# Performance work log

Measured on AMD Instinct MI355X. Metric: run time of the kernel, lower is better.

## Reference

```python
import jax, jax.numpy as jnp
import numpy as np

NUM_HEADS = 16
BUDGET = 1024


def layer_norm(x, g, b, eps=1e-5):
    mu = jnp.mean(x, axis=-1, keepdims=True)
    var = jnp.mean((x - mu) ** 2, axis=-1, keepdims=True)
    return (x - mu) / jnp.sqrt(var + eps) * g + b


def setup_inputs() -> dict:
    key = jax.random.key(0)
    ks = jax.random.split(key, 6)
    B, N, D = 2, 2048, 1024
    H, Dh = NUM_HEADS, 1024 // NUM_HEADS
    sc = 1.0 / np.sqrt(D).astype(np.float32)
    X = jax.random.normal(ks[0], (B, N, D), jnp.float32)
    W_q = jax.random.normal(ks[1], (D, D), jnp.float32) * sc
    W_k = jax.random.normal(ks[2], (D, D), jnp.float32) * sc
    W_v = jax.random.normal(ks[3], (D, D), jnp.float32) * sc
    W_o = jax.random.normal(ks[4], (D, D), jnp.float32) * sc
    return dict(
        X=X, W_q=W_q, W_k=W_k, W_v=W_v, W_o=W_o,
        gamma_q=jnp.ones((D,), jnp.float32), beta_q=jnp.zeros((D,), jnp.float32),
        gamma_k=jnp.ones((D,), jnp.float32), beta_k=jnp.zeros((D,), jnp.float32),
        cache_k=jnp.zeros((B, H, BUDGET, Dh), jnp.float32),
        cache_v=jnp.zeros((B, H, BUDGET, Dh), jnp.float32),
        start_pos=0,
    )


def reference(X, W_q, W_k, W_v, W_o, gamma_q, beta_q, gamma_k, beta_k,
              cache_k, cache_v, start_pos):
    B, N, D = X.shape
    H = NUM_HEADS
    Dh = D // H
    budget = cache_k.shape[2]
    M = start_pos + N  # total kv length

    XQ = layer_norm(X @ W_q, gamma_q, beta_q).reshape(B, N, H, Dh).transpose(0, 2, 1, 3)
    XK = layer_norm(X @ W_k, gamma_k, beta_k).reshape(B, N, H, Dh).transpose(0, 2, 1, 3)
    XV = (X @ W_v).reshape(B, N, H, Dh).transpose(0, 2, 1, 3)

    K = jnp.concatenate([cache_k[:B, :, :start_pos], XK], axis=2)  # (B,H,M,Dh)
    V = jnp.concatenate([cache_v[:B, :, :start_pos], XV], axis=2)

    logits = jnp.einsum('bhnd,bhmd->bhnm', XQ, K) / np.float32(np.sqrt(Dh))
    n_idx = jnp.arange(N)[:, None]
    m_idx = jnp.arange(M)[None, :]
    causal_keep = (m_idx < start_pos) | ((m_idx - start_pos) <= n_idx)  # (N,M)
    logits = jnp.where(causal_keep, logits, -jnp.inf)

    # --- selection (eviction) scores from head 0 ---
    S = jax.nn.relu(logits[:, 0])                        # (B,N,M); relu(-inf)=0
    S = S.at[:, :, start_pos].set(0.0)                   # never evict <BOS>-like slot
    S = S.at[:, :, start_pos:].multiply(1.0 - jnp.eye(N, dtype=S.dtype))  # zero diagonal
    S = jnp.roll(S, 1, axis=1).at[:, 0, :].set(0.0)      # shift: scores apply from next query
    Fm = jnp.cumsum(S, axis=1)                           # (B,N,M) cumulative eviction scores

    # --- sequential heavy-hitter eviction ---
    unmasked0 = jnp.broadcast_to(jnp.arange(budget, dtype=jnp.int32), (B, budget))
    kpos = jnp.arange(budget, dtype=jnp.int32)[None, :]

    def step(unmasked, i):
        new_idx = jnp.concatenate(
            [unmasked, jnp.full((B, 1), i, unmasked.dtype)], axis=1)     # (B,budget+1)
        row = jax.lax.dynamic_index_in_dim(Fm, i - start_pos, axis=1, keepdims=False)  # (B,M)
        scores = jnp.take_along_axis(row, new_idx, axis=1)
        idx = jnp.argmax(scores, axis=-1)                                # (B,)
        evicted = jnp.take_along_axis(new_idx, idx[:, None], axis=1)[:, 0]
        unmasked = jnp.where(kpos < idx[:, None], new_idx[:, :budget], new_idx[:, 1:])
        return unmasked, evicted

    steps = jnp.arange(max(budget, start_pos), M, dtype=jnp.int32)       # (T,)
    _, evicts = jax.lax.scan(step, unmasked0, steps)                     # evicts (T,B)

    big = jnp.int32(M + start_pos + 1)
    evict_time = jnp.full((B, M), big, jnp.int32)
    evict_time = evict_time.at[jnp.arange(B, dtype=jnp.int32)[None, :], evicts].min(steps[:, None])
    # query row j is pruned from key m iff (j + start_pos) >= evict_time[m]
    prune_keep = (jnp.arange(N)[:, None] + start_pos) < evict_time[:, None, :]  # (B,N,M)

    logits = jnp.where(prune_keep[:, None], logits, -jnp.inf)
    attn = jax.nn.softmax(logits, axis=-1)
    O = jnp.einsum('bhnm,bhmd->bhnd', attn, V).transpose(0, 2, 1, 3).reshape(B, N, D)
    return O @ W_o
```

## Files before the change

kernel.cpp:

```cpp
#include <hip/hip_runtime.h>

#define B_    2
#define N_    2048
#define D_    1024
#define H_    16
#define DH_   64
#define M_    2048
#define ROWS_ 4096
#define BUD_  1024

typedef unsigned short u16;
typedef unsigned int   u32;
typedef unsigned long long u64;
typedef __attribute__((ext_vector_type(8))) short short8;
typedef __attribute__((ext_vector_type(4))) float floatx4;

__device__ __forceinline__ u16 f2b(float f) {
    u32 u = __float_as_uint(f);
    return (u16)((u + 0x7FFFu + ((u >> 16) & 1u)) >> 16);
}
__device__ __forceinline__ float b2f(u16 h) {
    return __uint_as_float(((u32)h) << 16);
}

__global__ __launch_bounds__(256) void cast_x_kernel(
    const float* __restrict__ X, u16* __restrict__ Xhi, u16* __restrict__ Xlo)
{
    int idx = (blockIdx.x * 256 + threadIdx.x) * 4;
    float4 v = *(const float4*)&X[idx];
    u16 h0 = f2b(v.x), h1 = f2b(v.y), h2 = f2b(v.z), h3 = f2b(v.w);
    ushort4 hv; hv.x = h0; hv.y = h1; hv.z = h2; hv.w = h3;
    *(ushort4*)&Xhi[idx] = hv;
    ushort4 lv;
    lv.x = f2b(v.x - b2f(h0)); lv.y = f2b(v.y - b2f(h1));
    lv.z = f2b(v.z - b2f(h2)); lv.w = f2b(v.w - b2f(h3));
    *(ushort4*)&Xlo[idx] = lv;
}

__global__ __launch_bounds__(1024) void cast_w_kernel(
    const float* __restrict__ W, u16* __restrict__ Whi, u16* __restrict__ Wlo,
    int do_lo)
{
    __shared__ float tile[32][33];
    int tx = threadIdx.x, ty = threadIdx.y;
    int x = blockIdx.x * 32 + tx, y = blockIdx.y * 32 + ty;
    tile[ty][tx] = W[(size_t)y * D_ + x];
    __syncthreads();
    float v = tile[tx][ty];
    int n = blockIdx.x * 32 + ty, k = blockIdx.y * 32 + tx;
    u16 h = f2b(v);
    Whi[(size_t)n * D_ + k] = h;
    if (do_lo) Wlo[(size_t)n * D_ + k] = f2b(v - b2f(h));
}

__global__ __launch_bounds__(256) void gemm_kernel(
    const u16* __restrict__ Ah, const u16* __restrict__ Al,
    const u16* __restrict__ Bh, const u16* __restrict__ Bl,
    int mode, float* __restrict__ C)
{
    __shared__ __align__(16) u16 sAh[128 * 32];
    __shared__ __align__(16) u16 sBh[128 * 32];
    __shared__ __align__(16) u16 sAl[128 * 32];
    __shared__ __align__(16) u16 sBl[128 * 32];
    int tid = threadIdx.x;
    int lane = tid & 63, wv = tid >> 6;
    int wr = wv >> 1, wc = wv & 1;
    int quad = lane >> 4, l16 = lane & 15;
    int m0 = blockIdx.y * 128, n0 = blockIdx.x * 128;

    floatx4 acc[4][4];
    floatx4 zero = {0.f, 0.f, 0.f, 0.f};
#pragma unroll
    for (int i = 0; i < 4; ++i)
#pragma unroll
        for (int j = 0; j < 4; ++j) acc[i][j] = zero;

    for (int k0 = 0; k0 < 1024; k0 += 32) {
#pragma unroll
        for (int it = 0; it < 2; ++it) {
            int e = (tid + it * 256) * 8;
            int r = e >> 5, c = e & 31;
            *(uint4*)&sAh[e] = *(const uint4*)&Ah[(size_t)(m0 + r) * 1024 + k0 + c];
            *(uint4*)&sBh[e] = *(const uint4*)&Bh[(size_t)(n0 + r) * 1024 + k0 + c];
            if (mode) {
                *(uint4*)&sAl[e] = *(const uint4*)&Al[(size_t)(m0 + r) * 1024 + k0 + c];
                *(uint4*)&sBl[e] = *(const uint4*)&Bl[(size_t)(n0 + r) * 1024 + k0 + c];
            }
        }
        __syncthreads();
        short8 ah[4], al[4], bh[4], bl[4];
#pragma unroll
        for (int x = 0; x < 4; ++x) {
            int ra = (wr * 64 + x * 16 + l16) * 32 + quad * 8;
            int rb = (wc * 64 + x * 16 + l16) * 32 + quad * 8;
            ah[x] = *(const short8*)&sAh[ra];
            bh[x] = *(const short8*)&sBh[rb];
            if (mode) {
                al[x] = *(const short8*)&sAl[ra];
                bl[x] = *(const short8*)&sBl[rb];
            }
        }
#pragma unroll
        for (int mi = 0; mi < 4; ++mi)
#pragma unroll
            for (int ni = 0; ni < 4; ++ni) {
                acc[mi][ni] = __builtin_amdgcn_mfma_f32_16x16x32_bf16(
                    ah[mi], bh[ni], acc[mi][ni], 0, 0, 0);
                if (mode) {
                    acc[mi][ni] = __builtin_amdgcn_mfma_f32_16x16x32_bf16(
                        ah[mi], bl[ni], acc[mi][ni], 0, 0, 0);
                    acc[mi][ni] = __builtin_amdgcn_mfma_f32_16x16x32_bf16(
                        al[mi], bh[ni], acc[mi][ni], 0, 0, 0);
                }
            }
        __syncthreads();
    }
#pragma unroll
    for (int mi = 0; mi < 4; ++mi)
#pragma unroll
        for (int ni = 0; ni < 4; ++ni)
#pragma unroll
            for (int r = 0; r < 4; ++r) {
                int row = m0 + wr * 64 + mi * 16 + quad * 4 + r;
                int col = n0 + wc * 64 + ni * 16 + l16;
                C[(size_t)row * 1024 + col] = acc[mi][ni][r];
            }
}

__global__ __launch_bounds__(256) void lnpack_kernel(
    const float* __restrict__ Y, const float* __restrict__ gamma,
    const float* __restrict__ beta, u16* __restrict__ Pk,
    float* __restrict__ head0, int do_ln)
{
    int r = blockIdx.x;
    int tid = threadIdx.x;
    float4 v = *(const float4*)&Y[(size_t)r * D_ + tid * 4];
    float mu = 0.f, rsig = 1.f;
    __shared__ float sS[4], sQ[4];
    if (do_ln) {
        float s = v.x + v.y + v.z + v.w;
        float q = v.x * v.x + v.y * v.y + v.z * v.z + v.w * v.w;
#pragma unroll
        for (int d = 1; d < 64; d <<= 1) { s += __shfl_xor(s, d); q += __shfl_xor(q, d); }
        if ((tid & 63) == 0) { sS[tid >> 6] = s; sQ[tid >> 6] = q; }
        __syncthreads();
        s = sS[0] + sS[1] + sS[2] + sS[3];
        q = sQ[0] + sQ[1] + sQ[2] + sQ[3];
        mu = s * (1.f / 1024.f);
        float var = q * (1.f / 1024.f) - mu * mu;
        rsig = rsqrtf(var + 1e-5f);
    }
    int b = r >> 11, n = r & 2047;
    float xs[4] = {v.x, v.y, v.z, v.w};
#pragma unroll
    for (int j = 0; j < 4; ++j) {
        int c = tid * 4 + j;
        float val = do_ln ? ((xs[j] - mu) * rsig * gamma[c] + beta[c]) : xs[j];
        int h = c >> 6, dh = c & 63;
        Pk[(((size_t)b * H_ + h) * N_ + n) * DH_ + dh] = f2b(val);
        if (head0 && c < 64) head0[(size_t)r * 64 + c] = val;
    }
}

__global__ void s_kernel(const float* __restrict__ q0,
                         const float* __restrict__ k0, float* __restrict__ S)
{
    int b = blockIdx.z;
    int n0 = blockIdx.y * 16, m0 = blockIdx.x * 16;
    int tx = threadIdx.x, ty = threadIdx.y;
    int n = n0 + ty, m = m0 + tx;
    float* out = S + ((size_t)b * N_ + n) * M_ + m;
    if (m0 > n0 + 15) { *out = 0.f; return; }
    __shared__ float sq[16][65], sk[16][65];
    int tid = ty * 16 + tx;
    {
        int rr = tid >> 4, cc = (tid & 15) * 4;
        float4 qa = *(const float4*)&q0[((size_t)b * N_ + n0 + rr) * 64 + cc];
        sq[rr][cc] = qa.x; sq[rr][cc + 1] = qa.y; sq[rr][cc + 2] = qa.z; sq[rr][cc + 3] = qa.w;
        float4 ka = *(const float4*)&k0[((size_t)b * N_ + m0 + rr) * 64 + cc];
        sk[rr][cc] = ka.x; sk[rr][cc + 1] = ka.y; sk[rr][cc + 2] = ka.z; sk[rr][cc + 3] = ka.w;
    }
    __syncthreads();
    float acc = 0.f;
#pragma unroll 8
    for (int d = 0; d < 64; ++d) acc += sq[ty][d] * sk[tx][d];
    float val;
    if (m < n && m != 0) val = fmaxf(acc * 0.125f, 0.f); else val = 0.f;
    *out = val;
}

__global__ __launch_bounds__(256) void p_kernel(const float* __restrict__ S,
                                                float* __restrict__ P)
{
    int b = blockIdx.z, c = blockIdx.y;
    int m = blockIdx.x * 256 + threadIdx.x;
    const float* base = S + ((size_t)b * N_ + c * 128) * M_ + m;
    float s = 0.f;
    for (int j = 0; j < 128; ++j) s += base[(size_t)j * M_];
    P[((size_t)b * 8 + c) * M_ + m] = s;
}

__device__ __forceinline__ void vsel(float& va, u32& la, float vb, u32 lb) {
    bool tk = vb > va;
    va = tk ? vb : va;
    la = tk ? lb : la;
}

template<int CTRL, int RMASK>
__device__ __forceinline__ void dpp_max_pack(float& v, u32& lo) {
    int hi = __float_as_int(v);
    int hi_o = __builtin_amdgcn_update_dpp(hi, hi, CTRL, RMASK, 0xF, false);
    int lo_o = __builtin_amdgcn_update_dpp((int)lo, (int)lo, CTRL, RMASK, 0xF, false);
    long long a = (long long)((((u64)(u32)hi) << 32) | lo);
    long long b = (long long)((((u64)(u32)hi_o) << 32) | (u32)lo_o);
    bool tk = b > a;
    v = tk ? __int_as_float(hi_o) : v;
    lo = tk ? (u32)lo_o : lo;
}

__device__ __forceinline__ void wave_argmax_to63(float& v, u32& lo) {
    dpp_max_pack<0x121, 0xF>(v, lo);
    dpp_max_pack<0x122, 0xF>(v, lo);
    dpp_max_pack<0x124, 0xF>(v, lo);
    dpp_max_pack<0x128, 0xF>(v, lo);
    dpp_max_pack<0x142, 0xA>(v, lo);
    dpp_max_pack<0x143, 0xC>(v, lo);
}

#define GLOAD(dst, voff, ptr, imm)                                    \
    asm volatile("global_load_dwordx4 %0, %1, %2 offset:" #imm        \
                 : "=v"(dst) : "v"(voff), "s"(ptr) : "memory")

#define ISSUE2(bank, row)                                             \
    {                                                                 \
        u32 r_ = (u32)((row) < 2047 ? (row) : 2047);                  \
        u32 vo = wbyte + r_ * 8192u;                                  \
        GLOAD(bank[0], vo, Sb, 0);                                    \
        GLOAD(bank[1], vo, Sb, 1024);                                 \
    }

#define VWAIT6()                                                      \
    do { asm volatile("s_waitcnt vmcnt(6)" ::: "memory");             \
         __builtin_amdgcn_sched_barrier(0); } while (0)
#define VWAIT0()                                                      \
    do { asm volatile("s_waitcnt vmcnt(0)" ::: "memory");             \
         __builtin_amdgcn_sched_barrier(0); } while (0)

__device__ __forceinline__ void evict_step4(
    int i, int t, int w, int par,
    const u32 (&lov)[2][4], float (&cum)[2][4], int (&evti)[2][4],
    const floatx4 (&bank)[2], uint2 (*spair)[4])
{
    const float NEGINF = __uint_as_float(0xFF800000u);
    float v0 = cum[0][0]; u32 l0 = lov[0][0];
    vsel(v0, l0, cum[0][1], lov[0][1]);
    float v1 = cum[0][2]; u32 l1 = lov[0][2];
    vsel(v1, l1, cum[0][3], lov[0][3]);
    vsel(v0, l0, v1, l1);
    float v2 = cum[1][0]; u32 l2 = lov[1][0];
    vsel(v2, l2, cum[1][1], lov[1][1]);
    float v3 = cum[1][2]; u32 l3 = lov[1][2];
    vsel(v3, l3, cum[1][3], lov[1][3]);
    vsel(v2, l2, v3, l3);
    vsel(v0, l0, v2, l2);
    wave_argmax_to63(v0, l0);
    if (t == 63) spair[par][w] = make_uint2(l0, (u32)__float_as_int(v0));
    asm volatile("s_waitcnt lgkmcnt(0)" ::: "memory");
    __builtin_amdgcn_sched_barrier(0);
    __builtin_amdgcn_s_barrier();
    __builtin_amdgcn_sched_barrier(0);
    uint2 q0 = spair[par][0], q1 = spair[par][1];
    uint2 q2 = spair[par][2], q3 = spair[par][3];
    long long k0 = (long long)((((u64)q0.y) << 32) | q0.x);
    long long k1 = (long long)((((u64)q1.y) << 32) | q1.x);
    long long k2 = (long long)((((u64)q2.y) << 32) | q2.x);
    long long k3 = (long long)((((u64)q3.y) << 32) | q3.x);
    long long ba = k0 > k1 ? k0 : k1;
    long long bb = k2 > k3 ? k2 : k3;
    long long bst = ba > bb ? ba : bb;
    const u32 lostar = (u32)(bst & 0xFFFFFFFFll);
#pragma unroll
    for (int c = 0; c < 2; ++c) {
        cum[c][0] += bank[c][0]; cum[c][1] += bank[c][1];
        cum[c][2] += bank[c][2]; cum[c][3] += bank[c][3];
    }
#pragma unroll
    for (int c = 0; c < 2; ++c)
#pragma unroll
        for (int e = 0; e < 4; ++e) {
            bool hit = (lov[c][e] == lostar);
            cum[c][e] = hit ? NEGINF : cum[c][e];
            evti[c][e] = hit ? i : evti[c][e];
        }
}

__device__ void evict_role(const float* __restrict__ S,
                           const float* __restrict__ P,
                           int* __restrict__ evt)
{
    int b = blockIdx.x;
    int tid = threadIdx.x;
    int w = tid >> 6, t = tid & 63;
    const float* Sb = S + (size_t)b * N_ * M_;
    int* evtb = evt + b * M_;
    const int mbase = 512 * w + 4 * t;
    const u32 wbyte = (u32)(2048 * w + 16 * t);
    __shared__ uint2 spair[2][4];
    u32 lov[2][4];
    int evti[2][4];
#pragma unroll
    for (int c = 0; c < 2; ++c)
#pragma unroll
        for (int e = 0; e < 4; ++e) {
            lov[c][e] = (u32)(2048 - (mbase + 256 * c + e));
            evti[c][e] = 0x3FFFFFFF;
        }
    float cum[2][4];
#pragma unroll
    for (int c = 0; c < 2; ++c) {
        float ax = 0.f, ay = 0.f, az = 0.f, aw = 0.f;
#pragma unroll
        for (int cc = 0; cc < 8; ++cc) {
            floatx4 pv = *(const floatx4*)&P[((size_t)b * 8 + cc) * M_ + mbase + 256 * c];
            ax += pv[0]; ay += pv[1]; az += pv[2]; aw += pv[3];
        }
        cum[c][0] = ax; cum[c][1] = ay; cum[c][2] = az; cum[c][3] = aw;
    }
    VWAIT0();
    floatx4 bA[2], bB[2], bC[2], bD[2];
    ISSUE2(bA, 1024)
    ISSUE2(bB, 1025)
    ISSUE2(bC, 1026)
    ISSUE2(bD, 1027)
#pragma unroll 1
    for (int ip = 1024; ip < 2048; ip += 4) {
        VWAIT6();
        evict_step4(ip + 0, t, w, 0, lov, cum, evti, bA, spair);
        ISSUE2(bA, ip + 4)
        VWAIT6();
        evict_step4(ip + 1, t, w, 1, lov, cum, evti, bB, spair);
        ISSUE2(bB, ip + 5)
        VWAIT6();
        evict_step4(ip + 2, t, w, 0, lov, cum, evti, bC, spair);
        ISSUE2(bC, ip + 6)
        VWAIT6();
        evict_step4(ip + 3, t, w, 1, lov, cum, evti, bD, spair);
        ISSUE2(bD, ip + 7)
    }
    VWAIT0();
#pragma unroll
    for (int c = 0; c < 2; ++c) {
        int4 o; o.x = evti[c][0]; o.y = evti[c][1];
        o.z = evti[c][2]; o.w = evti[c][3];
        *(int4*)&evtb[mbase + 256 * c] = o;
    }
}

__device__ void flash_role(
    const u16* __restrict__ Qb, const u16* __restrict__ Kb,
    const u16* __restrict__ Vb, const int* __restrict__ evtg,
    u16* __restrict__ Ob, int bh, int q0, int ktiles)
{
    int b = bh >> 4, h = bh & 15;
    int tid = threadIdx.x, lane = tid & 63, w = tid >> 6;
    int quad = lane >> 4, l16 = lane & 15;
    const u16* Qh = Qb + (size_t)bh * N_ * DH_;
    const u16* Kh = Kb + (size_t)bh * N_ * DH_;
    const u16* Vh = Vb + (size_t)bh * N_ * DH_;
    __shared__ __align__(16) u16 sK[64 * 64];
    __shared__ __align__(16) u16 sV[64 * 64];
    __shared__ __align__(16) u16 sP[4][16 * 64];
    __shared__ int sevt[64];

    short8 aq0 = *(const short8*)&Qh[(size_t)(q0 + w * 16 + l16) * 64 + quad * 8];
    short8 aq1 = *(const short8*)&Qh[(size_t)(q0 + w * 16 + l16) * 64 + quad * 8 + 32];

    floatx4 zero = {0.f, 0.f, 0.f, 0.f};
    floatx4 accO[4];
#pragma unroll
    for (int d = 0; d < 4; ++d) accO[d] = zero;
    float m_i[4] = {-1e30f, -1e30f, -1e30f, -1e30f};
    float l_i[4] = {0.f, 0.f, 0.f, 0.f};

    for (int kt = 0; kt < ktiles; ++kt) {
        int k0 = kt * 64;
#pragma unroll
        for (int it = 0; it < 2; ++it) {
            int e = (tid + it * 256) * 8;
            int r = e >> 6, c = e & 63;
            *(uint4*)&sK[e] = *(const uint4*)&Kh[(size_t)(k0 + r) * 64 + c];
            uint4 vv = *(const uint4*)&Vh[(size_t)(k0 + r) * 64 + c];
            sV[(c + 0) * 64 + r] = (u16)(vv.x & 0xFFFF);
            sV[(c + 1) * 64 + r] = (u16)(vv.x >> 16);
            sV[(c + 2) * 64 + r] = (u16)(vv.y & 0xFFFF);
            sV[(c + 3) * 64 + r] = (u16)(vv.y >> 16);
            sV[(c + 4) * 64 + r] = (u16)(vv.z & 0xFFFF);
            sV[(c + 5) * 64 + r] = (u16)(vv.z >> 16);
            sV[(c + 6) * 64 + r] = (u16)(vv.w & 0xFFFF);
            sV[(c + 7) * 64 + r] = (u16)(vv.w >> 16);
        }
        if (evtg && tid < 64) sevt[tid] = evtg[b * M_ + k0 + tid];
        __syncthreads();

        floatx4 lg[4];
        int nbase = q0 + w * 16 + quad * 4;
#pragma unroll
        for (int s = 0; s < 4; ++s) {
            floatx4 sc = zero;
            short8 bk0 = *(const short8*)&sK[(s * 16 + l16) * 64 + quad * 8];
            short8 bk1 = *(const short8*)&sK[(s * 16 + l16) * 64 + quad * 8 + 32];
            sc = __builtin_amdgcn_mfma_f32_16x16x32_bf16(aq0, bk0, sc, 0, 0, 0);
            sc = __builtin_amdgcn_mfma_f32_16x16x32_bf16(aq1, bk1, sc, 0, 0, 0);
            int m = k0 + s * 16 + l16;
            int ev = evtg ? sevt[s * 16 + l16] : 0x7FFFFFFF;
#pragma unroll
            for (int r = 0; r < 4; ++r) {
                int n = nbase + r;
                bool keep = (m <= n) && (n < ev);
                lg[s][r] = keep ? sc[r] * 0.125f : -1e30f;
            }
        }
        float mnew[4], scale[4], rs[4];
#pragma unroll
        for (int r = 0; r < 4; ++r) {
            float mx = fmaxf(fmaxf(lg[0][r], lg[1][r]), fmaxf(lg[2][r], lg[3][r]));
#pragma unroll
            for (int d = 1; d < 16; d <<= 1) mx = fmaxf(mx, __shfl_xor(mx, d));
            mnew[r] = fmaxf(m_i[r], mx);
            scale[r] = __expf(m_i[r] - mnew[r]);
            m_i[r] = mnew[r];
            rs[r] = 0.f;
        }
#pragma unroll
        for (int s = 0; s < 4; ++s)
#pragma unroll
            for (int r = 0; r < 4; ++r) {
                float p = __expf(lg[s][r] - mnew[r]);
                rs[r] += p;
                sP[w][(quad * 4 + r) * 64 + s * 16 + l16] = f2b(p);
            }
#pragma unroll
        for (int r = 0; r < 4; ++r) {
            float t_ = rs[r];
#pragma unroll
            for (int d = 1; d < 16; d <<= 1) t_ += __shfl_xor(t_, d);
            l_i[r] = l_i[r] * scale[r] + t_;
        }
#pragma unroll
        for (int dd = 0; dd < 4; ++dd) {
            accO[dd][0] *= scale[0]; accO[dd][1] *= scale[1];
            accO[dd][2] *= scale[2]; accO[dd][3] *= scale[3];
        }
        short8 ap0 = *(const short8*)&sP[w][l16 * 64 + quad * 8];
        short8 ap1 = *(const short8*)&sP[w][l16 * 64 + quad * 8 + 32];
#pragma unroll
        for (int dd = 0; dd < 4; ++dd) {
            short8 bv0 = *(const short8*)&sV[(dd * 16 + l16) * 64 + quad * 8];
            short8 bv1 = *(const short8*)&sV[(dd * 16 + l16) * 64 + quad * 8 + 32];
            accO[dd] = __builtin_amdgcn_mfma_f32_16x16x32_bf16(ap0, bv0, accO[dd], 0, 0, 0);
            accO[dd] = __builtin_amdgcn_mfma_f32_16x16x32_bf16(ap1, bv1, accO[dd], 0, 0, 0);
        }
        __syncthreads();
    }
#pragma unroll
    for (int dd = 0; dd < 4; ++dd)
#pragma unroll
        for (int r = 0; r < 4; ++r) {
            int n = q0 + w * 16 + quad * 4 + r;
            int col = h * 64 + dd * 16 + l16;
            Ob[((size_t)b * N_ + n) * D_ + col] = f2b(accO[dd][r] / l_i[r]);
        }
}

__global__ __launch_bounds__(256) void fused_evict_flash1(
    const float* __restrict__ S, const float* __restrict__ P,
    int* __restrict__ evt,
    const u16* __restrict__ Qb, const u16* __restrict__ Kb,
    const u16* __restrict__ Vb, u16* __restrict__ Ob)
{
    if (blockIdx.x < 2) {
        evict_role(S, P, evt);
    } else {
        int fid = blockIdx.x - 2;
        int bh = fid >> 4, j = fid & 15;
        flash_role(Qb, Kb, Vb, nullptr, Ob, bh, j * 64, j + 1);
    }
}

__global__ __launch_bounds__(256) void flash2_kernel(
    const u16* __restrict__ Qb, const u16* __restrict__ Kb,
    const u16* __restrict__ Vb, const int* __restrict__ evt,
    u16* __restrict__ Ob)
{
    int j = blockIdx.x + 16;
    flash_role(Qb, Kb, Vb, evt, Ob, blockIdx.y, j * 64, j + 1);
}

extern "C" void kernel_launch(void* const* d_in, const int* in_sizes, int n_in,
                              void* d_out, int out_size, void* d_ws, size_t ws_size,
                              hipStream_t stream)
{
    (void)in_sizes; (void)n_in; (void)out_size; (void)ws_size;
    const float* X  = (const float*)d_in[0];
    const float* Wq = (const float*)d_in[1];
    const float* Wk = (const float*)d_in[2];
    const float* Wv = (const float*)d_in[3];
    const float* Wo = (const float*)d_in[4];
    const float* gq = (const float*)d_in[5];
    const float* bq = (const float*)d_in[6];
    const float* gk = (const float*)d_in[7];
    const float* bk = (const float*)d_in[8];

    char* p = (char*)d_ws;
    const size_t SZ_XH = (size_t)ROWS_ * D_ * 2;
    const size_t SZ_W  = (size_t)D_ * D_ * 2;
    const size_t SZ_Y  = (size_t)ROWS_ * D_ * 4;
    const size_t SZ_PK = (size_t)ROWS_ * D_ * 2;
    const size_t SZ_H0 = (size_t)ROWS_ * 64 * 4;

    size_t o = 0;
    u16* Xhi = (u16*)(p + o); o += SZ_XH;
    u16* Xlo = (u16*)(p + o); o += SZ_XH;
    u16* Wqh = (u16*)(p + o); o += SZ_W;
    u16* Wql = (u16*)(p + o); o += SZ_W;
    u16* Wkh = (u16*)(p + o); o += SZ_W;
    u16* Wkl = (u16*)(p + o); o += SZ_W;
    u16* Wvh = (u16*)(p + o); o += SZ_W;
    u16* Woh = (u16*)(p + o); o += SZ_W;
    float* Yq = (float*)(p + o); size_t oYq = o; o += SZ_Y;
    float* Yk = (float*)(p + o); o += SZ_Y;
    float* Yv = (float*)(p + o); o += SZ_Y;
    u16* Qb = (u16*)(p + o); o += SZ_PK;
    u16* Kb = (u16*)(p + o); o += SZ_PK;
    u16* Vb = (u16*)(p + o); o += SZ_PK;
    float* q0s = (float*)(p + o); o += SZ_H0;
    float* k0s = (float*)(p + o); o += SZ_H0;
    float* Pp  = (float*)(p + o); o += (size_t)B_ * 8 * M_ * 4;
    int* evt   = (int*)(p + o);  o += (size_t)B_ * M_ * 4;
    float* S = (float*)(p + oYq);
    u16* Ob  = Xhi;

    cast_x_kernel<<<ROWS_ * D_ / (256 * 4), 256, 0, stream>>>(X, Xhi, Xlo);
    dim3 wgrid(32, 32), wblk(32, 32);
    cast_w_kernel<<<wgrid, wblk, 0, stream>>>(Wq, Wqh, Wql, 1);
    cast_w_kernel<<<wgrid, wblk, 0, stream>>>(Wk, Wkh, Wkl, 1);
    cast_w_kernel<<<wgrid, wblk, 0, stream>>>(Wv, Wvh, nullptr, 0);
    cast_w_kernel<<<wgrid, wblk, 0, stream>>>(Wo, Woh, nullptr, 0);

    dim3 ggrid(D_ / 128, ROWS_ / 128);
    gemm_kernel<<<ggrid, 256, 0, stream>>>(Xhi, Xlo, Wqh, Wql, 1, Yq);
    gemm_kernel<<<ggrid, 256, 0, stream>>>(Xhi, Xlo, Wkh, Wkl, 1, Yk);
    gemm_kernel<<<ggrid, 256, 0, stream>>>(Xhi, nullptr, Wvh, nullptr, 0, Yv);

    lnpack_kernel<<<ROWS_, 256, 0, stream>>>(Yq, gq, bq, Qb, q0s, 1);
    lnpack_kernel<<<ROWS_, 256, 0, stream>>>(Yk, gk, bk, Kb, k0s, 1);
    lnpack_kernel<<<ROWS_, 256, 0, stream>>>(Yv, nullptr, nullptr, Vb, nullptr, 0);

    s_kernel<<<dim3(M_ / 16, N_ / 16, B_), dim3(16, 16), 0, stream>>>(q0s, k0s, S);
    p_kernel<<<dim3(M_ / 256, 8, B_), 256, 0, stream>>>(S, Pp);

    fused_evict_flash1<<<514, 256, 0, stream>>>(S, Pp, evt, Qb, Kb, Vb, Ob);
    flash2_kernel<<<dim3(16, B_ * H_), 256, 0, stream>>>(Qb, Kb, Vb, evt, Ob);

    gemm_kernel<<<ggrid, 256, 0, stream>>>(Ob, nullptr, Woh, nullptr, 0, (float*)d_out);
}
```

Before: 844.6 us.

## Overlap half of output projection with flash2, retile score kernel, template GEMM mode

Output-projection rows whose attention results are finished after the first flash pass now run as extra blocks inside the second flash launch, and the remaining rows run in a smaller follow-up GEMM. The head-0 score kernel moves from one output per thread to a 64x64 tile with 4x4 register blocking and vector stores. The GEMM mode becomes a template parameter, so the split-precision branches and unused shared memory are compiled out. This adds launch-order dependencies on Ob rows and more code complexity.

```diff
diff --git a/kernel.cpp b/kernel.cpp
--- a/kernel.cpp
+++ b/kernel.cpp
@@ -53,20 +53,21 @@
     if (do_lo) Wlo[(size_t)n * D_ + k] = f2b(v - b2f(h));
 }
 
-__global__ __launch_bounds__(256) void gemm_kernel(
+template<int MODE>
+__device__ void gemm_core(
     const u16* __restrict__ Ah, const u16* __restrict__ Al,
     const u16* __restrict__ Bh, const u16* __restrict__ Bl,
-    int mode, float* __restrict__ C)
+    float* __restrict__ C, int bx, int m0)
 {
     __shared__ __align__(16) u16 sAh[128 * 32];
     __shared__ __align__(16) u16 sBh[128 * 32];
-    __shared__ __align__(16) u16 sAl[128 * 32];
-    __shared__ __align__(16) u16 sBl[128 * 32];
+    __shared__ __align__(16) u16 sAl[MODE ? 128 * 32 : 8];
+    __shared__ __align__(16) u16 sBl[MODE ? 128 * 32 : 8];
     int tid = threadIdx.x;
     int lane = tid & 63, wv = tid >> 6;
     int wr = wv >> 1, wc = wv & 1;
     int quad = lane >> 4, l16 = lane & 15;
-    int m0 = blockIdx.y * 128, n0 = blockIdx.x * 128;
+    int n0 = bx * 128;
 
     floatx4 acc[4][4];
     floatx4 zero = {0.f, 0.f, 0.f, 0.f};
@@ -82,7 +83,7 @@
             int r = e >> 5, c = e & 31;
             *(uint4*)&sAh[e] = *(const uint4*)&Ah[(size_t)(m0 + r) * 1024 + k0 + c];
             *(uint4*)&sBh[e] = *(const uint4*)&Bh[(size_t)(n0 + r) * 1024 + k0 + c];
-            if (mode) {
+            if (MODE) {
                 *(uint4*)&sAl[e] = *(const uint4*)&Al[(size_t)(m0 + r) * 1024 + k0 + c];
                 *(uint4*)&sBl[e] = *(const uint4*)&Bl[(size_t)(n0 + r) * 1024 + k0 + c];
             }
@@ -95,7 +96,7 @@
             int rb = (wc * 64 + x * 16 + l16) * 32 + quad * 8;
             ah[x] = *(const short8*)&sAh[ra];
             bh[x] = *(const short8*)&sBh[rb];
-            if (mode) {
+            if (MODE) {
                 al[x] = *(const short8*)&sAl[ra];
                 bl[x] = *(const short8*)&sBl[rb];
             }
@@ -106,7 +107,7 @@
             for (int ni = 0; ni < 4; ++ni) {
                 acc[mi][ni] = __builtin_amdgcn_mfma_f32_16x16x32_bf16(
                     ah[mi], bh[ni], acc[mi][ni], 0, 0, 0);
-                if (mode) {
+                if (MODE) {
                     acc[mi][ni] = __builtin_amdgcn_mfma_f32_16x16x32_bf16(
                         ah[mi], bl[ni], acc[mi][ni], 0, 0, 0);
                     acc[mi][ni] = __builtin_amdgcn_mfma_f32_16x16x32_bf16(
@@ -125,6 +126,17 @@
                 int col = n0 + wc * 64 + ni * 16 + l16;
                 C[(size_t)row * 1024 + col] = acc[mi][ni][r];
             }
+}
+
+template<int MODE>
+__global__ __launch_bounds__(256) void gemm_kernel_t(
+    const u16* __restrict__ Ah, const u16* __restrict__ Al,
+    const u16* __restrict__ Bh, const u16* __restrict__ Bl,
+    float* __restrict__ C, int ymode)
+{
+    int by = blockIdx.y;
+    int yidx = (ymode == 0) ? by : ((by < 8) ? by + 8 : by + 16);
+    gemm_core<MODE>(Ah, Al, Bh, Bl, C, blockIdx.x, yidx * 128);
 }
 
 __global__ __launch_bounds__(256) void lnpack_kernel(
@@ -162,31 +174,67 @@
     }
 }
 
-__global__ void s_kernel(const float* __restrict__ q0,
-                         const float* __restrict__ k0, float* __restrict__ S)
+__global__ __launch_bounds__(256) void s64_kernel(
+    const float* __restrict__ q0, const float* __restrict__ k0,
+    float* __restrict__ S)
 {
     int b = blockIdx.z;
-    int n0 = blockIdx.y * 16, m0 = blockIdx.x * 16;
-    int tx = threadIdx.x, ty = threadIdx.y;
-    int n = n0 + ty, m = m0 + tx;
-    float* out = S + ((size_t)b * N_ + n) * M_ + m;
-    if (m0 > n0 + 15) { *out = 0.f; return; }
-    __shared__ float sq[16][65], sk[16][65];
-    int tid = ty * 16 + tx;
+    int n0 = blockIdx.y * 64, m0 = blockIdx.x * 64;
+    int tid = threadIdx.x;
+    int tx = tid & 15, ty = tid >> 4;
+    floatx4 zero = {0.f, 0.f, 0.f, 0.f};
+    if (m0 > n0 + 63) {
+#pragma unroll
+        for (int i = 0; i < 4; ++i) {
+            int n = n0 + 4 * ty + i;
+            *(floatx4*)&S[((size_t)b * N_ + n) * M_ + m0 + 4 * tx] = zero;
+        }
+        return;
+    }
+    __shared__ float sq[64][65], sk[64][65];
     {
-        int rr = tid >> 4, cc = (tid & 15) * 4;
-        float4 qa = *(const float4*)&q0[((size_t)b * N_ + n0 + rr) * 64 + cc];
-        sq[rr][cc] = qa.x; sq[rr][cc + 1] = qa.y; sq[rr][cc + 2] = qa.z; sq[rr][cc + 3] = qa.w;
-        float4 ka = *(const float4*)&k0[((size_t)b * N_ + m0 + rr) * 64 + cc];
-        sk[rr][cc] = ka.x; sk[rr][cc + 1] = ka.y; sk[rr][cc + 2] = ka.z; sk[rr][cc + 3] = ka.w;
+        int r = tid >> 2, cseg = (tid & 3) * 16;
+        const float* qrow = &q0[((size_t)b * N_ + n0 + r) * 64 + cseg];
+        const float* krow = &k0[((size_t)b * N_ + m0 + r) * 64 + cseg];
+#pragma unroll
+        for (int u = 0; u < 4; ++u) {
+            float4 qa = *(const float4*)&qrow[u * 4];
+            sq[r][cseg + u * 4 + 0] = qa.x; sq[r][cseg + u * 4 + 1] = qa.y;
+            sq[r][cseg + u * 4 + 2] = qa.z; sq[r][cseg + u * 4 + 3] = qa.w;
+            float4 ka = *(const float4*)&krow[u * 4];
+            sk[r][cseg + u * 4 + 0] = ka.x; sk[r][cseg + u * 4 + 1] = ka.y;
+            sk[r][cseg + u * 4 + 2] = ka.z; sk[r][cseg + u * 4 + 3] = ka.w;
+        }
     }
     __syncthreads();
-    float acc = 0.f;
+    float acc[4][4];
+#pragma unroll
+    for (int i = 0; i < 4; ++i)
+#pragma unroll
+        for (int j = 0; j < 4; ++j) acc[i][j] = 0.f;
 #pragma unroll 8
-    for (int d = 0; d < 64; ++d) acc += sq[ty][d] * sk[tx][d];
-    float val;
-    if (m < n && m != 0) val = fmaxf(acc * 0.125f, 0.f); else val = 0.f;
-    *out = val;
+    for (int d = 0; d < 64; ++d) {
+        float qv[4], kv[4];
+#pragma unroll
+        for (int i = 0; i < 4; ++i) qv[i] = sq[4 * ty + i][d];
+#pragma unroll
+        for (int j = 0; j < 4; ++j) kv[j] = sk[4 * tx + j][d];
+#pragma unroll
+        for (int i = 0; i < 4; ++i)
+#pragma unroll
+            for (int j = 0; j < 4; ++j) acc[i][j] += qv[i] * kv[j];
+    }
+#pragma unroll
+    for (int i = 0; i < 4; ++i) {
+        int n = n0 + 4 * ty + i;
+        floatx4 out;
+#pragma unroll
+        for (int j = 0; j < 4; ++j) {
+            int m = m0 + 4 * tx + j;
+            out[j] = (m < n && m != 0) ? fmaxf(acc[i][j] * 0.125f, 0.f) : 0.f;
+        }
+        *(floatx4*)&S[((size_t)b * N_ + n) * M_ + m0 + 4 * tx] = out;
+    }
 }
 
 __global__ __launch_bounds__(256) void p_kernel(const float* __restrict__ S,
@@ -487,13 +535,22 @@
     }
 }
 
-__global__ __launch_bounds__(256) void flash2_kernel(
+__global__ __launch_bounds__(256) void fused_flash2_gemmo1(
     const u16* __restrict__ Qb, const u16* __restrict__ Kb,
     const u16* __restrict__ Vb, const int* __restrict__ evt,
-    u16* __restrict__ Ob)
-{
-    int j = blockIdx.x + 16;
-    flash_role(Qb, Kb, Vb, evt, Ob, blockIdx.y, j * 64, j + 1);
+    u16* __restrict__ Ob, const u16* __restrict__ Woh,
+    float* __restrict__ Out)
+{
+    if (blockIdx.x < 512) {
+        int fid = blockIdx.x;
+        int bh = fid >> 4, j = (fid & 15) + 16;
+        flash_role(Qb, Kb, Vb, evt, Ob, bh, j * 64, j + 1);
+    } else {
+        int gid = blockIdx.x - 512;
+        int bx = gid & 7, gy = gid >> 3;
+        int yidx = (gy < 8) ? gy : gy + 8;
+        gemm_core<0>((const u16*)Ob, nullptr, Woh, nullptr, Out, bx, yidx * 128);
+    }
 }
 
 extern "C" void kernel_launch(void* const* d_in, const int* in_sizes, int n_in,
@@ -548,19 +605,20 @@
     cast_w_kernel<<<wgrid, wblk, 0, stream>>>(Wo, Woh, nullptr, 0);
 
     dim3 ggrid(D_ / 128, ROWS_ / 128);
-    gemm_kernel<<<ggrid, 256, 0, stream>>>(Xhi, Xlo, Wqh, Wql, 1, Yq);
-    gemm_kernel<<<ggrid, 256, 0, stream>>>(Xhi, Xlo, Wkh, Wkl, 1, Yk);
-    gemm_kernel<<<ggrid, 256, 0, stream>>>(Xhi, nullptr, Wvh, nullptr, 0, Yv);
+    gemm_kernel_t<1><<<ggrid, 256, 0, stream>>>(Xhi, Xlo, Wqh, Wql, Yq, 0);
+    gemm_kernel_t<1><<<ggrid, 256, 0, stream>>>(Xhi, Xlo, Wkh, Wkl, Yk, 0);
+    gemm_kernel_t<0><<<ggrid, 256, 0, stream>>>(Xhi, nullptr, Wvh, nullptr, Yv, 0);
 
     lnpack_kernel<<<ROWS_, 256, 0, stream>>>(Yq, gq, bq, Qb, q0s, 1);
     lnpack_kernel<<<ROWS_, 256, 0, stream>>>(Yk, gk, bk, Kb, k0s, 1);
     lnpack_kernel<<<ROWS_, 256, 0, stream>>>(Yv, nullptr, nullptr, Vb, nullptr, 0);
 
-    s_kernel<<<dim3(M_ / 16, N_ / 16, B_), dim3(16, 16), 0, stream>>>(q0s, k0s, S);
+    s64_kernel<<<dim3(M_ / 64, N_ / 64, B_), 256, 0, stream>>>(q0s, k0s, S);
     p_kernel<<<dim3(M_ / 256, 8, B_), 256, 0, stream>>>(S, Pp);
 
     fused_evict_flash1<<<514, 256, 0, stream>>>(S, Pp, evt, Qb, Kb, Vb, Ob);
-    flash2_kernel<<<dim3(16, B_ * H_), 256, 0, stream>>>(Qb, Kb, Vb, evt, Ob);
-
-    gemm_kernel<<<ggrid, 256, 0, stream>>>(Ob, nullptr, Woh, nullptr, 0, (float*)d_out);
-}
+    fused_flash2_gemmo1<<<640, 256, 0, stream>>>(
+        Qb, Kb, Vb, evt, Ob, Woh, (float*)d_out);
+    gemm_kernel_t<0><<<dim3(8, 16), 256, 0, stream>>>(
+        (const u16*)Ob, nullptr, Woh, nullptr, (float*)d_out, 2);
+}
```

Result: faster. 812.6 us (-3.8%).
